# Performance work log

Measured on AMD Instinct MI355X. Metric: run time of the kernel, lower is better.

The kernel has to match this reference:

```python
import jax, jax.numpy as jnp
import numpy as np

CHANNELS = 256
LAYERS = 4
IN_FEAT = 118
N_NODES = 20000
N_EDGES = 320000


def setup_inputs() -> dict:
    key = jax.random.key(0)
    ks = jax.random.split(key, 4 + 4 * LAYERS)
    x = jax.random.normal(ks[0], (N_NODES, IN_FEAT), dtype=jnp.float32)
    edge_index = jax.random.randint(ks[1], (2, N_EDGES), 0, N_NODES, dtype=jnp.int64)
    s = 1.0 / np.sqrt(CHANNELS)
    W_embed = jax.random.normal(ks[2], (IN_FEAT, CHANNELS), dtype=jnp.float32) / np.sqrt(IN_FEAT)
    b_embed = jnp.zeros((CHANNELS,), dtype=jnp.float32)
    W1 = jax.random.normal(ks[3], (LAYERS, CHANNELS, CHANNELS), dtype=jnp.float32) * s
    b1 = jnp.zeros((LAYERS, CHANNELS), dtype=jnp.float32)
    W2 = jax.random.normal(ks[4], (LAYERS, CHANNELS, CHANNELS), dtype=jnp.float32) * s
    b2 = jnp.zeros((LAYERS, CHANNELS), dtype=jnp.float32)
    return {"x": x, "edge_index": edge_index, "W_embed": W_embed, "b_embed": b_embed,
            "W1": W1, "b1": b1, "W2": W2, "b2": b2}


def reference(x, edge_index, W_embed, b_embed, W1, b1, W2, b2):
    n = x.shape[0]
    src, dst = edge_index[0], edge_index[1]
    # in-degree for mean aggregation (constant across layers)
    cnt = jax.ops.segment_sum(jnp.ones(src.shape[0], dtype=x.dtype), dst, num_segments=n)
    inv_cnt = (1.0 / jnp.maximum(cnt, 1.0))[:, None]
    h = x @ W_embed + b_embed  # [N, C]
    for l in range(W1.shape[0]):
        # message: gather source features, dense + exact GELU (dropout off in eval)
        msg = jax.nn.gelu(h[src] @ W1[l] + b1[l], approximate=False)  # [E, C]
        # mean-scatter aggregate over destination nodes
        agg = jax.ops.segment_sum(msg, dst, num_segments=n) * inv_cnt  # [N, C]
        # update: dense + GELU
        h = jax.nn.gelu(agg @ W2[l] + b2[l], approximate=False)
    return jnp.mean(h, axis=1)  # [N]
```

## Files before the change

### kernel.cpp

```cpp
#include <hip/hip_runtime.h>
#include <math.h>
#include <stdint.h>

#define CH 256

typedef _Float16 half8 __attribute__((ext_vector_type(8)));
typedef _Float16 half4 __attribute__((ext_vector_type(4)));
typedef float f32x4 __attribute__((ext_vector_type(4)));

__device__ __forceinline__ float gelu_exact(float v) {
    return 0.5f * v * (1.0f + erff(v * 0.70710678118654752f));
}

__global__ void wsplit_kernel(const float* __restrict__ W1, const float* __restrict__ W2,
                              _Float16* __restrict__ WThi, _Float16* __restrict__ WTlo) {
    int idx = blockIdx.x * blockDim.x + threadIdx.x;
    int n   = idx & 255;
    int kg  = (idx >> 8) & 31;
    int mat = idx >> 13;
    const float* W = (mat < 4) ? (W1 + (size_t)mat * 65536)
                               : (W2 + (size_t)(mat - 4) * 65536);
    _Float16 hi[8], lo[8];
#pragma unroll
    for (int j = 0; j < 8; j++) {
        float v = W[(size_t)(kg * 8 + j) * CH + n];
        _Float16 h = (_Float16)v;
        hi[j] = h;
        lo[j] = (_Float16)(v - (float)h);
    }
    size_t off = (size_t)mat * 65536 + ((size_t)(kg >> 2) * 256 + n) * 32 + (kg & 3) * 8;
    *(half8*)(WThi + off) = *(half8*)&hi[0];
    *(half8*)(WTlo + off) = *(half8*)&lo[0];
}

__global__ void wesplit_kernel(const float* __restrict__ We,
                               _Float16* __restrict__ WeTh, _Float16* __restrict__ WeTl) {
    int idx = blockIdx.x * blockDim.x + threadIdx.x;
    if (idx >= 4096) return;
    int n  = idx >> 4;
    int k8 = (idx & 15) * 8;
    _Float16 hi[8], lo[8];
#pragma unroll
    for (int j = 0; j < 8; j++) {
        int k = k8 + j;
        float v = (k < 118) ? We[(size_t)k * CH + n] : 0.f;
        _Float16 h = (_Float16)v;
        hi[j] = h;
        lo[j] = (_Float16)(v - (float)h);
    }
    size_t off = ((size_t)(k8 >> 5) * 256 + n) * 32 + (k8 & 31);
    *(half8*)(WeTh + off) = *(half8*)&hi[0];
    *(half8*)(WeTl + off) = *(half8*)&lo[0];
}

__global__ void xsplit_kernel(const float* __restrict__ x,
                              _Float16* __restrict__ xh, _Float16* __restrict__ xl,
                              int N, int Mpad) {
    int idx = blockIdx.x * blockDim.x + threadIdx.x;
    int n  = idx >> 4;
    int c8 = (idx & 15) * 8;
    if (n >= N) return;
    _Float16 hi[8], lo[8];
#pragma unroll
    for (int j = 0; j < 8; j++) {
        int c = c8 + j;
        float v = (c < 118) ? x[(size_t)n * 118 + c] : 0.f;
        _Float16 h = (_Float16)v;
        hi[j] = h;
        lo[j] = (_Float16)(v - (float)h);
    }
    size_t off = ((size_t)(c8 >> 5) * Mpad + n) * 32 + (c8 & 31);
    *(half8*)(xh + off) = *(half8*)&hi[0];
    *(half8*)(xl + off) = *(half8*)&lo[0];
}

template<int KT, bool DOGELU, bool TILED>
__global__ __launch_bounds__(256, 4) void mgemm_kernel(
    const _Float16* __restrict__ Ah_g, const _Float16* __restrict__ Al_g,
    const _Float16* __restrict__ Bh_g, const _Float16* __restrict__ Bl_g,
    const float* __restrict__ bias,
    _Float16* __restrict__ Oh, _Float16* __restrict__ Ol,
    int Mpad, int MC)
{
    __shared__ __align__(16) char smem[30720];
    _Float16 (*Ah)[40] = (_Float16(*)[40])smem;
    _Float16 (*Al)[40] = (_Float16(*)[40])(smem + 10240);
    _Float16 (*Bh)[40] = (_Float16(*)[40])(smem + 20480);
    _Float16 (*Bl)[40] = (_Float16(*)[40])(smem + 25600);
    uint32_t (*Obuf)[68] = (uint32_t(*)[68])smem;

    int b    = blockIdx.x;
    int xcd  = b & 7;
    int slot = b >> 3;
    int mt   = xcd * MC + (slot >> 2);
    int nt   = slot & 3;
    if (mt * 128 >= Mpad) return;
    int m0 = mt * 128;
    int n0 = nt * 64;

    int tid  = threadIdx.x;
    int lane = tid & 63;
    int wave = tid >> 6;
    int wr = wave >> 1;
    int wc = wave & 1;

    f32x4 acc[4][2];
#pragma unroll
    for (int i = 0; i < 4; i++)
#pragma unroll
        for (int j = 0; j < 2; j++) acc[i][j] = (f32x4){0.f, 0.f, 0.f, 0.f};

    const int Lb    = tid * 8;
    const int arow0 = Lb >> 5;
    const int ak    = Lb & 31;

    for (int kt = 0; kt < KT; kt++) {
        const _Float16* pah = Ah_g + ((size_t)kt * Mpad + m0) * 32;
        const _Float16* pal = Al_g + ((size_t)kt * Mpad + m0) * 32;
        const _Float16* pbh = Bh_g + ((size_t)kt * 256 + n0) * 32;
        const _Float16* pbl = Bl_g + ((size_t)kt * 256 + n0) * 32;
        half8 a0 = *(const half8*)(pah + Lb);
        half8 a1 = *(const half8*)(pah + 2048 + Lb);
        half8 a2 = *(const half8*)(pal + Lb);
        half8 a3 = *(const half8*)(pal + 2048 + Lb);
        half8 b0 = *(const half8*)(pbh + Lb);
        half8 b1 = *(const half8*)(pbl + Lb);
        *(half8*)&Ah[arow0][ak]      = a0;
        *(half8*)&Ah[64 + arow0][ak] = a1;
        *(half8*)&Al[arow0][ak]      = a2;
        *(half8*)&Al[64 + arow0][ak] = a3;
        *(half8*)&Bh[arow0][ak]      = b0;
        *(half8*)&Bl[arow0][ak]      = b1;
        __syncthreads();

        {
            int frow = lane & 15;
            int fk   = (lane >> 4) * 8;
            half8 ah[4], al[4], bh[2], bl[2];
#pragma unroll
            for (int rf = 0; rf < 4; rf++) {
                int r = wr * 64 + rf * 16 + frow;
                ah[rf] = *(const half8*)&Ah[r][fk];
                al[rf] = *(const half8*)&Al[r][fk];
            }
#pragma unroll
            for (int cf = 0; cf < 2; cf++) {
                int c = wc * 32 + cf * 16 + frow;
                bh[cf] = *(const half8*)&Bh[c][fk];
                bl[cf] = *(const half8*)&Bl[c][fk];
            }
#pragma unroll
            for (int rf = 0; rf < 4; rf++)
#pragma unroll
                for (int cf = 0; cf < 2; cf++) {
                    acc[rf][cf] = __builtin_amdgcn_mfma_f32_16x16x32_f16(ah[rf], bh[cf], acc[rf][cf], 0, 0, 0);
                    acc[rf][cf] = __builtin_amdgcn_mfma_f32_16x16x32_f16(ah[rf], bl[cf], acc[rf][cf], 0, 0, 0);
                    acc[rf][cf] = __builtin_amdgcn_mfma_f32_16x16x32_f16(al[rf], bh[cf], acc[rf][cf], 0, 0, 0);
                }
        }
        __syncthreads();
    }

    int ccol = lane & 15;
    int crow = (lane >> 4) * 4;
    float bb[2];
    bb[0] = bias[n0 + wc * 32 + ccol];
    bb[1] = bias[n0 + wc * 32 + 16 + ccol];
#pragma unroll
    for (int half = 0; half < 2; half++) {
        if (wr == half) {
#pragma unroll
            for (int cf = 0; cf < 2; cf++)
#pragma unroll
                for (int rf = 0; rf < 4; rf++)
#pragma unroll
                    for (int q = 0; q < 4; q++) {
                        float v = acc[rf][cf][q] + bb[cf];
                        float g = DOGELU ? gelu_exact(v) : v;
                        _Float16 hi = (_Float16)g;
                        _Float16 lo = (_Float16)(g - (float)hi);
                        uint32_t u = (uint32_t)__builtin_bit_cast(uint16_t, hi)
                                   | ((uint32_t)__builtin_bit_cast(uint16_t, lo) << 16);
                        Obuf[rf * 16 + crow + q][wc * 32 + cf * 16 + ccol] = u;
                    }
        }
        __syncthreads();
#pragma unroll
        for (int i = 0; i < 8; i++) {
            int idx = i * 512 + tid * 2;
            int row = idx >> 6;
            int c   = idx & 63;
            uint32_t u0 = Obuf[row][c];
            uint32_t u1 = Obuf[row][c + 1];
            uint32_t hi2 = (u0 & 0xffffu) | (u1 << 16);
            uint32_t lo2 = (u0 >> 16) | (u1 & 0xffff0000u);
            int grow = m0 + half * 64 + row;
            int gcol = n0 + c;
            size_t off = TILED ? ((size_t)(gcol >> 5) * Mpad + grow) * 32 + (gcol & 31)
                               : (size_t)grow * CH + gcol;
            *(uint32_t*)(Oh + off) = hi2;
            *(uint32_t*)(Ol + off) = lo2;
        }
        __syncthreads();
    }
}

__global__ void zero_int_kernel(int* p, int n) {
    int i = blockIdx.x * blockDim.x + threadIdx.x;
    if (i < n) p[i] = 0;
}

__global__ void degree_kernel(const int* __restrict__ ei, int E, int* deg) {
    int e = blockIdx.x * blockDim.x + threadIdx.x;
    if (e < E) atomicAdd(&deg[ei[E + e]], 1);
}

__global__ void scan_part_kernel(const int* __restrict__ deg, int* bsum, int N) {
    int t = threadIdx.x;
    int base = blockIdx.x * 1024 + t * 4;
    int4 v = {0, 0, 0, 0};
    if (base + 3 < N) v = *(const int4*)(deg + base);
    else {
        if (base + 0 < N) v.x = deg[base + 0];
        if (base + 1 < N) v.y = deg[base + 1];
        if (base + 2 < N) v.z = deg[base + 2];
        if (base + 3 < N) v.w = deg[base + 3];
    }
    __shared__ int sh[256];
    sh[t] = v.x + v.y + v.z + v.w;
    __syncthreads();
    for (int off = 128; off; off >>= 1) {
        if (t < off) sh[t] += sh[t + off];
        __syncthreads();
    }
    if (t == 0) bsum[blockIdx.x] = sh[0];
}

__global__ void scan_top_kernel(const int* __restrict__ bsum, int* boff, int B) {
    __shared__ int sh[256];
    int t = threadIdx.x;
    int own = (t < B) ? bsum[t] : 0;
    sh[t] = own;
    __syncthreads();
    for (int off = 1; off < 256; off <<= 1) {
        int v = (t >= off) ? sh[t - off] : 0;
        __syncthreads();
        sh[t] += v;
        __syncthreads();
    }
    if (t < B) boff[t] = sh[t] - own;
}

__global__ void scan_final_kernel(const int* __restrict__ deg, const int* __restrict__ boff,
                                  int* row_ptr, int* fill_pos, float* inv, int N, int E) {
    int t = threadIdx.x;
    int base = blockIdx.x * 1024 + t * 4;
    int4 v = {0, 0, 0, 0};
    if (base + 3 < N) v = *(const int4*)(deg + base);
    else {
        if (base + 0 < N) v.x = deg[base + 0];
        if (base + 1 < N) v.y = deg[base + 1];
        if (base + 2 < N) v.z = deg[base + 2];
        if (base + 3 < N) v.w = deg[base + 3];
    }
    int own = v.x + v.y + v.z + v.w;
    __shared__ int sh[256];
    sh[t] = own;
    __syncthreads();
    for (int off = 1; off < 256; off <<= 1) {
        int s = (t >= off) ? sh[t - off] : 0;
        __syncthreads();
        sh[t] += s;
        __syncthreads();
    }
    int run = boff[blockIdx.x] + (sh[t] - own);
    int4 rp;
    rp.x = run;
    rp.y = run + v.x;
    rp.z = rp.y + v.y;
    rp.w = rp.z + v.z;
    if (base + 3 < N) {
        *(int4*)(row_ptr + base) = rp;
        *(int4*)(fill_pos + base) = rp;
        float4 iv;
        iv.x = 1.0f / fmaxf((float)v.x, 1.0f);
        iv.y = 1.0f / fmaxf((float)v.y, 1.0f);
        iv.z = 1.0f / fmaxf((float)v.z, 1.0f);
        iv.w = 1.0f / fmaxf((float)v.w, 1.0f);
        *(float4*)(inv + base) = iv;
    } else {
        int rr[4] = {rp.x, rp.y, rp.z, rp.w};
        int dd[4] = {v.x, v.y, v.z, v.w};
        for (int q = 0; q < 4; q++) {
            if (base + q < N) {
                row_ptr[base + q] = rr[q];
                fill_pos[base + q] = rr[q];
                inv[base + q] = 1.0f / fmaxf((float)dd[q], 1.0f);
            }
        }
    }
    if (blockIdx.x == 0 && t == 0) row_ptr[N] = E;
}

__global__ void fill_kernel(const int* __restrict__ ei, int E, int* fill_pos, int* colv) {
    int e = blockIdx.x * blockDim.x + threadIdx.x;
    if (e < E) {
        int p = atomicAdd(&fill_pos[ei[E + e]], 1);
        colv[p] = ei[e];
    }
}

__global__ void agg_kernel(const _Float16* __restrict__ th, const _Float16* __restrict__ tl,
                           const int* __restrict__ row_ptr, const int* __restrict__ colv,
                           const float* __restrict__ inv,
                           _Float16* __restrict__ aggh, _Float16* __restrict__ aggl,
                           int N, int Mpad) {
    int n = blockIdx.x * 4 + (threadIdx.x >> 6);
    if (n >= N) return;
    int lane = threadIdx.x & 63;
    int s = row_ptr[n], e = row_ptr[n + 1];
    size_t loff = (size_t)lane * 4;

    f32x4 a0 = {0.f, 0.f, 0.f, 0.f}, a1 = a0, a2 = a0, a3 = a0;
    int j = s;
    for (; j + 4 <= e; j += 4) {
        int c0 = colv[j], c1 = colv[j + 1], c2 = colv[j + 2], c3 = colv[j + 3];
        half4 h0 = *(const half4*)(th + (size_t)c0 * CH + loff);
        half4 l0 = *(const half4*)(tl + (size_t)c0 * CH + loff);
        half4 h1 = *(const half4*)(th + (size_t)c1 * CH + loff);
        half4 l1 = *(const half4*)(tl + (size_t)c1 * CH + loff);
        half4 h2 = *(const half4*)(th + (size_t)c2 * CH + loff);
        half4 l2 = *(const half4*)(tl + (size_t)c2 * CH + loff);
        half4 h3 = *(const half4*)(th + (size_t)c3 * CH + loff);
        half4 l3 = *(const half4*)(tl + (size_t)c3 * CH + loff);
#pragma unroll
        for (int q = 0; q < 4; q++) {
            a0[q] += (float)h0[q] + (float)l0[q];
            a1[q] += (float)h1[q] + (float)l1[q];
            a2[q] += (float)h2[q] + (float)l2[q];
            a3[q] += (float)h3[q] + (float)l3[q];
        }
    }
    for (; j < e; j++) {
        int c = colv[j];
        half4 h = *(const half4*)(th + (size_t)c * CH + loff);
        half4 l = *(const half4*)(tl + (size_t)c * CH + loff);
#pragma unroll
        for (int q = 0; q < 4; q++) a0[q] += (float)h[q] + (float)l[q];
    }
    f32x4 tot = (a0 + a1) + (a2 + a3);
    float sc = inv[n];
    _Float16 oh[4], ol[4];
#pragma unroll
    for (int q = 0; q < 4; q++) {
        float v = tot[q] * sc;
        _Float16 hi = (_Float16)v;
        oh[q] = hi;
        ol[q] = (_Float16)(v - (float)hi);
    }
    size_t ooff = ((size_t)(lane >> 3) * Mpad + n) * 32 + ((lane * 4) & 31);
    *(half4*)(aggh + ooff) = *(half4*)&oh[0];
    *(half4*)(aggl + ooff) = *(half4*)&ol[0];
}

__global__ void mean_kernel(const _Float16* __restrict__ hh, const _Float16* __restrict__ hl,
                            float* __restrict__ out, int N, int Mpad) {
    int n = blockIdx.x * 4 + (threadIdx.x >> 6);
    if (n >= N) return;
    int lane = threadIdx.x & 63;
    size_t off = ((size_t)(lane >> 3) * Mpad + n) * 32 + ((lane * 4) & 31);
    half4 vh = *(const half4*)(hh + off);
    half4 vl = *(const half4*)(hl + off);
    float s = 0.f;
#pragma unroll
    for (int q = 0; q < 4; q++) s += (float)vh[q] + (float)vl[q];
#pragma unroll
    for (int off2 = 32; off2; off2 >>= 1) s += __shfl_down(s, off2, 64);
    if (lane == 0) out[n] = s * (1.0f / 256.0f);
}

extern "C" void kernel_launch(void* const* d_in, const int* in_sizes, int n_in,
                              void* d_out, int out_size, void* d_ws, size_t ws_size,
                              hipStream_t stream) {
    const float* x       = (const float*)d_in[0];
    const int*   ei      = (const int*)d_in[1];
    const float* W_embed = (const float*)d_in[2];
    const float* b_embed = (const float*)d_in[3];
    const float* W1      = (const float*)d_in[4];
    const float* b1      = (const float*)d_in[5];
    const float* W2      = (const float*)d_in[6];
    const float* b2      = (const float*)d_in[7];
    float* out = (float*)d_out;

    int N = in_sizes[0] / 118;
    int E = in_sizes[1] / 2;
    int SB = (N + 1023) / 1024;
    int Mpad = ((N + 127) / 128) * 128;
    size_t NC = (size_t)Mpad * CH;

    _Float16* hh   = (_Float16*)d_ws;
    _Float16* hl   = hh + NC;
    _Float16* th   = hl + NC;
    _Float16* tl   = th + NC;
    _Float16* ah   = tl + NC;
    _Float16* al   = ah + NC;
    _Float16* WThi = al + NC;
    _Float16* WTlo = WThi + 8 * 65536;
    _Float16* WeTh = WTlo + 8 * 65536;
    _Float16* WeTl = WeTh + 32768;
    float*    inv      = (float*)(WeTl + 32768);
    int*      deg      = (int*)(inv + N);
    int*      row_ptr  = deg + N;
    int*      fill_pos = row_ptr + (N + 1);
    int*      colv     = fill_pos + N;
    int*      bsum     = colv + E;
    int*      boff     = bsum + 256;

    _Float16* xh = th;
    _Float16* xl = th + (size_t)Mpad * 128;

    zero_int_kernel<<<(N + 255) / 256, 256, 0, stream>>>(deg, N);
    degree_kernel<<<(E + 255) / 256, 256, 0, stream>>>(ei, E, deg);
    scan_part_kernel<<<SB, 256, 0, stream>>>(deg, bsum, N);
    scan_top_kernel<<<1, 256, 0, stream>>>(bsum, boff, SB);
    scan_final_kernel<<<SB, 256, 0, stream>>>(deg, boff, row_ptr, fill_pos, inv, N, E);
    fill_kernel<<<(E + 255) / 256, 256, 0, stream>>>(ei, E, fill_pos, colv);
    wsplit_kernel<<<256, 256, 0, stream>>>(W1, W2, WThi, WTlo);
    wesplit_kernel<<<16, 256, 0, stream>>>(W_embed, WeTh, WeTl);
    xsplit_kernel<<<(N * 16 + 255) / 256, 256, 0, stream>>>(x, xh, xl, N, Mpad);

    int mtiles = Mpad / 128;
    int MC = (mtiles + 7) / 8;
    int mgrid = 8 * MC * 4;

    mgemm_kernel<4, false, true><<<mgrid, 256, 0, stream>>>(xh, xl, WeTh, WeTl, b_embed,
                                                            hh, hl, Mpad, MC);
    for (int l = 0; l < 4; l++) {
        mgemm_kernel<8, true, false><<<mgrid, 256, 0, stream>>>(hh, hl,
                                                                WThi + (size_t)l * 65536,
                                                                WTlo + (size_t)l * 65536,
                                                                b1 + (size_t)l * CH,
                                                                th, tl, Mpad, MC);
        agg_kernel<<<(N + 3) / 4, 256, 0, stream>>>(th, tl, row_ptr, colv, inv,
                                                    ah, al, N, Mpad);
        mgemm_kernel<8, true, true><<<mgrid, 256, 0, stream>>>(ah, al,
                                                               WThi + (size_t)(4 + l) * 65536,
                                                               WTlo + (size_t)(4 + l) * 65536,
                                                               b2 + (size_t)l * CH,
                                                               hh, hl, Mpad, MC);
    }
    mean_kernel<<<(N + 3) / 4, 256, 0, stream>>>(hh, hl, out, N, Mpad);
}
```

Baseline: 428.2 us.

## Interleave hi/lo halves in message buffer and slice aggregation by column blocks

The non-tiled GEMM output now stores each element's hi and lo fp16 halves packed together in one 32-bit word, in a single buffer, instead of two separate arrays. The aggregation kernel reads one packed word per lane per neighbor. Its grid is split into 8 column slices of 32 channels, with 8 nodes per block and 32 lanes per node. This halves the number of gather load streams and keeps each slice's working set smaller, which may improve L2 locality. The cost is many more blocks, narrower 4-byte loads per lane, and each neighbor index being re-read once per slice.

New measurement: 435.6 us. No clear change (+1.7%).

```diff
diff --git a/kernel.cpp b/kernel.cpp
--- a/kernel.cpp
+++ b/kernel.cpp
@@ -10,6 +10,12 @@
 
 __device__ __forceinline__ float gelu_exact(float v) {
     return 0.5f * v * (1.0f + erff(v * 0.70710678118654752f));
+}
+
+__device__ __forceinline__ float upk(uint32_t u) {
+    _Float16 h = __builtin_bit_cast(_Float16, (uint16_t)(u & 0xffffu));
+    _Float16 l = __builtin_bit_cast(_Float16, (uint16_t)(u >> 16));
+    return (float)h + (float)l;
 }
 
 __global__ void wsplit_kernel(const float* __restrict__ W1, const float* __restrict__ W2,
@@ -192,14 +198,18 @@
             int c   = idx & 63;
             uint32_t u0 = Obuf[row][c];
             uint32_t u1 = Obuf[row][c + 1];
-            uint32_t hi2 = (u0 & 0xffffu) | (u1 << 16);
-            uint32_t lo2 = (u0 >> 16) | (u1 & 0xffff0000u);
             int grow = m0 + half * 64 + row;
             int gcol = n0 + c;
-            size_t off = TILED ? ((size_t)(gcol >> 5) * Mpad + grow) * 32 + (gcol & 31)
-                               : (size_t)grow * CH + gcol;
-            *(uint32_t*)(Oh + off) = hi2;
-            *(uint32_t*)(Ol + off) = lo2;
+            if (TILED) {
+                uint32_t hi2 = (u0 & 0xffffu) | (u1 << 16);
+                uint32_t lo2 = (u0 >> 16) | (u1 & 0xffff0000u);
+                size_t off = ((size_t)(gcol >> 5) * Mpad + grow) * 32 + (gcol & 31);
+                *(uint32_t*)(Oh + off) = hi2;
+                *(uint32_t*)(Ol + off) = lo2;
+            } else {
+                uint2 pk; pk.x = u0; pk.y = u1;
+                *(uint2*)((uint32_t*)Oh + (size_t)grow * CH + gcol) = pk;
+            }
         }
         __syncthreads();
     }
@@ -310,57 +320,40 @@
     }
 }
 
-__global__ void agg_kernel(const _Float16* __restrict__ th, const _Float16* __restrict__ tl,
-                           const int* __restrict__ row_ptr, const int* __restrict__ colv,
-                           const float* __restrict__ inv,
-                           _Float16* __restrict__ aggh, _Float16* __restrict__ aggl,
-                           int N, int Mpad) {
-    int n = blockIdx.x * 4 + (threadIdx.x >> 6);
+__global__ __launch_bounds__(256) void agg_kernel(
+    const uint32_t* __restrict__ tpk,
+    const int* __restrict__ row_ptr, const int* __restrict__ colv,
+    const float* __restrict__ inv,
+    _Float16* __restrict__ aggh, _Float16* __restrict__ aggl,
+    int N, int Mpad)
+{
+    int b = blockIdx.x;
+    int slice = b & 7;
+    int n = (b >> 3) * 8 + (threadIdx.x >> 5);
     if (n >= N) return;
-    int lane = threadIdx.x & 63;
+    int lane = threadIdx.x & 31;
+    const uint32_t* base = tpk + slice * 32 + lane;
+
     int s = row_ptr[n], e = row_ptr[n + 1];
-    size_t loff = (size_t)lane * 4;
-
-    f32x4 a0 = {0.f, 0.f, 0.f, 0.f}, a1 = a0, a2 = a0, a3 = a0;
+    float a0 = 0.f, a1 = 0.f, a2 = 0.f, a3 = 0.f;
     int j = s;
     for (; j + 4 <= e; j += 4) {
         int c0 = colv[j], c1 = colv[j + 1], c2 = colv[j + 2], c3 = colv[j + 3];
-        half4 h0 = *(const half4*)(th + (size_t)c0 * CH + loff);
-        half4 l0 = *(const half4*)(tl + (size_t)c0 * CH + loff);
-        half4 h1 = *(const half4*)(th + (size_t)c1 * CH + loff);
-        half4 l1 = *(const half4*)(tl + (size_t)c1 * CH + loff);
-        half4 h2 = *(const half4*)(th + (size_t)c2 * CH + loff);
-        half4 l2 = *(const half4*)(tl + (size_t)c2 * CH + loff);
-        half4 h3 = *(const half4*)(th + (size_t)c3 * CH + loff);
-        half4 l3 = *(const half4*)(tl + (size_t)c3 * CH + loff);
-#pragma unroll
-        for (int q = 0; q < 4; q++) {
-            a0[q] += (float)h0[q] + (float)l0[q];
-            a1[q] += (float)h1[q] + (float)l1[q];
-            a2[q] += (float)h2[q] + (float)l2[q];
-            a3[q] += (float)h3[q] + (float)l3[q];
-        }
-    }
-    for (; j < e; j++) {
-        int c = colv[j];
-        half4 h = *(const half4*)(th + (size_t)c * CH + loff);
-        half4 l = *(const half4*)(tl + (size_t)c * CH + loff);
-#pragma unroll
-        for (int q = 0; q < 4; q++) a0[q] += (float)h[q] + (float)l[q];
-    }
-    f32x4 tot = (a0 + a1) + (a2 + a3);
-    float sc = inv[n];
-    _Float16 oh[4], ol[4];
-#pragma unroll
-    for (int q = 0; q < 4; q++) {
-        float v = tot[q] * sc;
-        _Float16 hi = (_Float16)v;
-        oh[q] = hi;
-        ol[q] = (_Float16)(v - (float)hi);
-    }
-    size_t ooff = ((size_t)(lane >> 3) * Mpad + n) * 32 + ((lane * 4) & 31);
-    *(half4*)(aggh + ooff) = *(half4*)&oh[0];
-    *(half4*)(aggl + ooff) = *(half4*)&ol[0];
+        uint32_t u0 = base[(size_t)c0 * CH];
+        uint32_t u1 = base[(size_t)c1 * CH];
+        uint32_t u2 = base[(size_t)c2 * CH];
+        uint32_t u3 = base[(size_t)c3 * CH];
+        a0 += upk(u0); a1 += upk(u1); a2 += upk(u2); a3 += upk(u3);
+    }
+    for (; j < e; j++)
+        a0 += upk(base[(size_t)colv[j] * CH]);
+
+    float v = ((a0 + a1) + (a2 + a3)) * inv[n];
+    _Float16 hi = (_Float16)v;
+    _Float16 lo = (_Float16)(v - (float)hi);
+    size_t ooff = ((size_t)slice * Mpad + n) * 32 + lane;
+    aggh[ooff] = hi;
+    aggl[ooff] = lo;
 }
 
 __global__ void mean_kernel(const _Float16* __restrict__ hh, const _Float16* __restrict__ hl,
@@ -416,6 +409,7 @@
     int*      bsum     = colv + E;
     int*      boff     = bsum + 256;
 
+    uint32_t* tpk = (uint32_t*)th;
     _Float16* xh = th;
     _Float16* xl = th + (size_t)Mpad * 128;
 
@@ -432,6 +426,7 @@
     int mtiles = Mpad / 128;
     int MC = (mtiles + 7) / 8;
     int mgrid = 8 * MC * 4;
+    int agrid = 8 * ((N + 7) / 8);
 
     mgemm_kernel<4, false, true><<<mgrid, 256, 0, stream>>>(xh, xl, WeTh, WeTl, b_embed,
                                                             hh, hl, Mpad, MC);
@@ -440,9 +435,9 @@
                                                                 WThi + (size_t)l * 65536,
                                                                 WTlo + (size_t)l * 65536,
                                                                 b1 + (size_t)l * CH,
-                                                                th, tl, Mpad, MC);
-        agg_kernel<<<(N + 3) / 4, 256, 0, stream>>>(th, tl, row_ptr, colv, inv,
-                                                    ah, al, N, Mpad);
+                                                                (_Float16*)tpk, nullptr,
+                                                                Mpad, MC);
+        agg_kernel<<<agrid, 256, 0, stream>>>(tpk, row_ptr, colv, inv, ah, al, N, Mpad);
         mgemm_kernel<8, true, true><<<mgrid, 256, 0, stream>>>(ah, al,
                                                                WThi + (size_t)(4 + l) * 65536,
                                                                WTlo + (size_t)(4 + l) * 65536,
```
